# Kernel optimization log

Measured on AMD Instinct MI355X. Metric: run time of the kernel, lower is better.

Reference implementation:

```python
import jax, jax.numpy as jnp
import numpy as np

B, N, OBS, H, S, A, K = 65536, 10, 64, 50, 10, 2, 2  # batch, agents, obs_dim, hidden, comm symbols, actions, k_steps
NEG = -1e9


def setup_inputs() -> dict:
    key = jax.random.key(0)
    ks = jax.random.split(key, 12)
    def lin(k, fan_in, shape):
        return (jax.random.uniform(k, shape, jnp.float32, -1.0, 1.0) / np.sqrt(fan_in).astype(np.float32))
    IN_F = H + S + H  # hidden + comm + skip(h0) = 110
    return {
        "obs": jax.random.normal(ks[0], (B, N, OBS), jnp.float32),
        "mask": jnp.ones((B, N), jnp.float32),
        "W_enc": lin(ks[1], OBS, (OBS, H)),
        "b_enc": lin(ks[2], OBS, (H,)),
        "W_f": lin(ks[3], IN_F, (K, IN_F, H)),
        "b_f": lin(ks[4], IN_F, (K, H)),
        "W_comm": lin(ks[5], H, (H, S)),
        "b_comm": lin(ks[6], H, (S,)),
        "W_pi": lin(ks[7], H, (H, A)),
        "b_pi": lin(ks[8], H, (A,)),
        "W_v": lin(ks[9], H, (H, 1)),
        "b_v": lin(ks[10], H, (1,)),
    }


def reference(obs, mask, W_enc, b_enc, W_f, b_f, W_comm, b_comm, W_pi, b_pi, W_v, b_v):
    mask3 = mask[..., None]                      # [B,N,1]
    h0 = jnp.tanh(obs @ W_enc + b_enc)           # [B,N,H]
    h = h0
    comm_logp = jnp.zeros(obs.shape[:2], obs.dtype)  # [B,N]
    c = jnp.zeros((*obs.shape[:2], S), obs.dtype)
    for i in range(K):  # k_steps is small & static
        comm_logits = h @ W_comm + b_comm        # [B,N,S]
        masked = jnp.where(mask3 == 0, NEG, comm_logits)
        logp = jax.nn.log_softmax(masked, axis=-1)
        w = jnp.argmax(masked, axis=-1)          # greedy symbol per agent [B,N]
        comm_logp = comm_logp + jnp.take_along_axis(logp, w[..., None], axis=-1)[..., 0] * mask
        w_onehot = jax.nn.one_hot(w, S, dtype=obs.dtype)  # [B,N,S]
        # bag-of-words OR aggregation across agents, broadcast back to every agent
        c = jnp.clip(jnp.sum(w_onehot, axis=1, keepdims=True), 0.0, 1.0)  # [B,1,S]
        c = jnp.broadcast_to(c, w_onehot.shape)  # [B,N,S]
        inp = jnp.concatenate([h, c, h0], axis=-1)  # [B,N,H+S+H]
        h = jnp.tanh(inp @ W_f[i] + b_f[i])
    logits = h @ W_pi + b_pi                      # [B,N,A]
    logits = jnp.where(mask3 == 0, NEG, logits)
    baseline = (h @ W_v + b_v)[..., 0] * mask     # [B,N]
    return logits, baseline, comm_logp, c
```

## Files before the change

kernel.cpp:

```cpp
#include <hip/hip_runtime.h>
#include <math.h>

#define NAGENT 10
#define OBS_D  64
#define HID    50
#define NSYM   10
#define NACT   2
#define NEGV   (-1e9f)

#define BPB 6
#define TPB 64
#define AG  (BPB * NAGENT)

#define LD 52

#define OFF_WC0  3328
#define OFF_W1S  5928
#define OFF_W1H  8528
#define OFF_WC0c 11128
#define OFF_W1c  11648
#define NPREP    (234 * LD)

__device__ __forceinline__ float fast_tanh(float x) {
  float xc = fminf(15.f, fmaxf(-15.f, x));
  float e  = __expf(2.f * xc);
  return __fdividef(e - 1.f, e + 1.f);
}

__global__ void prep_weights(const float* __restrict__ W_enc,
                             const float* __restrict__ W_f,
                             float* __restrict__ ws) {
  int i = blockIdx.x * blockDim.x + threadIdx.x;
  if (i >= NPREP) return;
  int j = i % LD;
  int r = i / LD;
  float v = 0.f;
  if (j < HID) {
    if      (r <  64)                { v = W_enc[r*HID + j]; }
    else if (r < 114) { int k=r-64;    v = W_f[k*HID + j] + W_f[(60+k)*HID + j]; }
    else if (r < 164) { int k=r-114;   v = W_f[(110+60+k)*HID + j]; }
    else if (r < 214) { int k=r-164;   v = W_f[(110+k)*HID + j]; }
    else if (r < 224) { int s=r-214;   v = W_f[(50+s)*HID + j]; }
    else              { int s=r-224;   v = W_f[(110+50+s)*HID + j]; }
  }
  ws[i] = v;
}

__device__ __forceinline__ int comm_pick(float cl[NSYM], float mk, float& clp) {
  #pragma unroll
  for (int s = 0; s < NSYM; s++) cl[s] = (mk == 0.f) ? NEGV : cl[s];
  int w = 0; float best = cl[0];
  #pragma unroll
  for (int s = 1; s < NSYM; s++) { bool b = cl[s] > best; best = b ? cl[s] : best; w = b ? s : w; }
  float se = 0.f;
  #pragma unroll
  for (int s = 0; s < NSYM; s++) se += __expf(cl[s] - best);
  clp += (-__logf(se)) * mk;
  return w;
}

__global__ __launch_bounds__(TPB, 4) void policy_kernel(
    const float* __restrict__ obs,
    const float* __restrict__ mask,
    const float* __restrict__ b_enc,
    const float* __restrict__ b_f,
    const float* __restrict__ W_comm,
    const float* __restrict__ b_comm,
    const float* __restrict__ W_pi,
    const float* __restrict__ b_pi,
    const float* __restrict__ W_v,
    const float* __restrict__ b_v,
    const float* __restrict__ wsP,
    float* __restrict__ out,
    int B)
{
  __shared__ float hbuf[AG * 51];
  const int t   = threadIdx.x;
  const int be0 = blockIdx.x * BPB;
  const int nbe = min(BPB, B - be0);
  const int nag = nbe * NAGENT;
  const bool act = (t < nag);
  const int bel = t / NAGENT;
  const long long NA = (long long)B * NAGENT;
  const long long g  = (long long)be0 * NAGENT + t;
  const long long gc = act ? g : (NA - 1);
  const int sl = act ? t : 0;

  const float* WencP = wsP;
  const float* WC0   = wsP + OFF_WC0;
  const float* W1S   = wsP + OFF_W1S;
  const float* W1H   = wsP + OFF_W1H;
  const float* WC0c  = wsP + OFF_WC0c;
  const float* W1c   = wsP + OFF_W1c;

  const float mk = mask[gc];

  float acc[HID];
  #pragma unroll
  for (int j = 0; j < HID; j++) acc[j] = b_enc[j];
  {
    const float4* o4 = (const float4*)(obs + gc * OBS_D);
    #pragma unroll 2
    for (int k4 = 0; k4 < OBS_D / 4; k4++) {
      float4 v = o4[k4];
      const float* wr = &WencP[k4 * 4 * LD];
      #pragma unroll
      for (int j = 0; j < HID; j++) acc[j] = fmaf(v.x, wr[j], acc[j]);
      #pragma unroll
      for (int j = 0; j < HID; j++) acc[j] = fmaf(v.y, wr[LD + j], acc[j]);
      #pragma unroll
      for (int j = 0; j < HID; j++) acc[j] = fmaf(v.z, wr[2 * LD + j], acc[j]);
      #pragma unroll
      for (int j = 0; j < HID; j++) acc[j] = fmaf(v.w, wr[3 * LD + j], acc[j]);
    }
  }

  float cl[NSYM];
  #pragma unroll
  for (int s = 0; s < NSYM; s++) cl[s] = b_comm[s];
  if (act) {
    float* myh = &hbuf[t * 51];
    #pragma unroll
    for (int j = 0; j < HID; j++) {
      float h = fast_tanh(acc[j]);
      myh[j] = h;
      const float* wc = &W_comm[j * NSYM];
      #pragma unroll
      for (int s = 0; s < NSYM; s++) cl[s] = fmaf(h, wc[s], cl[s]);
    }
  }

  float clp = 0.f;

  int w = comm_pick(cl, mk, clp);
  const int sh = bel * NAGENT;
  float c_reg[NSYM];
  #pragma unroll
  for (int s = 0; s < NSYM; s++) {
    unsigned long long b = __ballot(w == s);
    c_reg[s] = ((b >> sh) & 0x3FFULL) ? 1.f : 0.f;
  }

  float pre1[HID];
  #pragma unroll
  for (int j = 0; j < HID; j++) acc[j]  = b_f[j];
  #pragma unroll
  for (int j = 0; j < HID; j++) pre1[j] = b_f[HID + j];
  {
    const float* myh = &hbuf[sl * 51];
    #pragma unroll 2
    for (int k = 0; k < HID; k++) {
      float x = myh[k];
      const float* w0 = &WC0[k * LD];
      const float* w1 = &W1S[k * LD];
      #pragma unroll
      for (int j = 0; j < HID; j++) acc[j]  = fmaf(x, w0[j], acc[j]);
      #pragma unroll
      for (int j = 0; j < HID; j++) pre1[j] = fmaf(x, w1[j], pre1[j]);
    }
  }
  #pragma unroll
  for (int s = 0; s < NSYM; s++) {
    float cv = c_reg[s];
    const float* wr = &WC0c[s * LD];
    #pragma unroll
    for (int j = 0; j < HID; j++) acc[j] = fmaf(cv, wr[j], acc[j]);
  }

  #pragma unroll
  for (int s = 0; s < NSYM; s++) cl[s] = b_comm[s];
  if (act) {
    float* myh = &hbuf[t * 51];
    #pragma unroll
    for (int j = 0; j < HID; j++) {
      float h = fast_tanh(acc[j]);
      myh[j] = h;
      const float* wc = &W_comm[j * NSYM];
      #pragma unroll
      for (int s = 0; s < NSYM; s++) cl[s] = fmaf(h, wc[s], cl[s]);
    }
  }

  w = comm_pick(cl, mk, clp);
  #pragma unroll
  for (int s = 0; s < NSYM; s++) {
    unsigned long long b = __ballot(w == s);
    c_reg[s] = ((b >> sh) & 0x3FFULL) ? 1.f : 0.f;
  }

  #pragma unroll
  for (int s = 0; s < NSYM; s++) {
    float cv = c_reg[s];
    const float* wr = &W1c[s * LD];
    #pragma unroll
    for (int j = 0; j < HID; j++) pre1[j] = fmaf(cv, wr[j], pre1[j]);
  }
  {
    const float* myh = &hbuf[sl * 51];
    #pragma unroll 2
    for (int k = 0; k < HID; k++) {
      float x = myh[k];
      const float* wr = &W1H[k * LD];
      #pragma unroll
      for (int j = 0; j < HID; j++) pre1[j] = fmaf(x, wr[j], pre1[j]);
    }
  }

  float l0 = b_pi[0], l1 = b_pi[1], bv = b_v[0];
  #pragma unroll
  for (int j = 0; j < HID; j++) {
    float h = fast_tanh(pre1[j]);
    l0 = fmaf(h, W_pi[j * NACT + 0], l0);
    l1 = fmaf(h, W_pi[j * NACT + 1], l1);
    bv = fmaf(h, W_v[j], bv);
  }

  if (act) {
    float2* o2 = (float2*)out;
    o2[g] = make_float2((mk == 0.f) ? NEGV : l0, (mk == 0.f) ? NEGV : l1);
    out[NA * 2 + g] = bv * mk;
    out[NA * 3 + g] = clp;
    float2* c2 = (float2*)(out + NA * 4);
    const long long cb = g * (NSYM / 2);
    #pragma unroll
    for (int s = 0; s < NSYM / 2; s++)
      c2[cb + s] = make_float2(c_reg[2 * s], c_reg[2 * s + 1]);
  }
}

extern "C" void kernel_launch(void* const* d_in, const int* in_sizes, int n_in,
                              void* d_out, int out_size, void* d_ws, size_t ws_size,
                              hipStream_t stream) {
  const float* obs    = (const float*)d_in[0];
  const float* mask   = (const float*)d_in[1];
  const float* W_enc  = (const float*)d_in[2];
  const float* b_enc  = (const float*)d_in[3];
  const float* W_f    = (const float*)d_in[4];
  const float* b_f    = (const float*)d_in[5];
  const float* W_comm = (const float*)d_in[6];
  const float* b_comm = (const float*)d_in[7];
  const float* W_pi   = (const float*)d_in[8];
  const float* b_pi   = (const float*)d_in[9];
  const float* W_v    = (const float*)d_in[10];
  const float* b_v    = (const float*)d_in[11];
  float* out = (float*)d_out;
  float* ws  = (float*)d_ws;

  const int B = in_sizes[0] / (NAGENT * OBS_D);

  hipLaunchKernelGGL(prep_weights, dim3((NPREP + 255) / 256), dim3(256), 0, stream,
                     W_enc, W_f, ws);

  const int grid = (B + BPB - 1) / BPB;
  hipLaunchKernelGGL(policy_kernel, dim3(grid), dim3(TPB), 0, stream,
                     obs, mask, b_enc, b_f, W_comm, b_comm, W_pi, b_pi, W_v, b_v,
                     ws, out, B);
}
```

Before: 535.1 us.

## Keep hidden state in registers, stash partial pre-activation in LDS, pad W_comm

The hidden vector h now stays in registers instead of going through shared memory. The partial second-layer pre-activation (h0 contribution) is computed early and parked in LDS, so only one 50-wide accumulator is live at a time. W_comm is re-laid out with padded rows in the workspace, and the obs loads are batched into 8 float4 per half. This is meant to cut LDS round trips and register pressure from holding two accumulators at once. In exchange it adds a block sync and fully unrolled loops, which could raise code size or spill.

After: 1.641 ms. 207% more time.

```diff
diff --git a/kernel.cpp b/kernel.cpp
--- a/kernel.cpp
+++ b/kernel.cpp
@@ -12,14 +12,16 @@
 #define TPB 64
 #define AG  (BPB * NAGENT)
 
-#define LD 52
+#define LD  52
+#define CLD 12
 
 #define OFF_WC0  3328
 #define OFF_W1S  5928
 #define OFF_W1H  8528
 #define OFF_WC0c 11128
 #define OFF_W1c  11648
-#define NPREP    (234 * LD)
+#define OFF_WCM  12168
+#define NPREP    (OFF_WCM + HID * CLD)
 
 __device__ __forceinline__ float fast_tanh(float x) {
   float xc = fminf(15.f, fmaxf(-15.f, x));
@@ -29,21 +31,27 @@
 
 __global__ void prep_weights(const float* __restrict__ W_enc,
                              const float* __restrict__ W_f,
+                             const float* __restrict__ W_comm,
                              float* __restrict__ ws) {
   int i = blockIdx.x * blockDim.x + threadIdx.x;
   if (i >= NPREP) return;
-  int j = i % LD;
-  int r = i / LD;
-  float v = 0.f;
-  if (j < HID) {
-    if      (r <  64)                { v = W_enc[r*HID + j]; }
-    else if (r < 114) { int k=r-64;    v = W_f[k*HID + j] + W_f[(60+k)*HID + j]; }
-    else if (r < 164) { int k=r-114;   v = W_f[(110+60+k)*HID + j]; }
-    else if (r < 214) { int k=r-164;   v = W_f[(110+k)*HID + j]; }
-    else if (r < 224) { int s=r-214;   v = W_f[(50+s)*HID + j]; }
-    else              { int s=r-224;   v = W_f[(110+50+s)*HID + j]; }
-  }
-  ws[i] = v;
+  if (i < OFF_WCM) {
+    int j = i % LD;
+    int r = i / LD;
+    float v = 0.f;
+    if (j < HID) {
+      if      (r <  64)                { v = W_enc[r*HID + j]; }
+      else if (r < 114) { int k=r-64;    v = W_f[k*HID + j] + W_f[(60+k)*HID + j]; }
+      else if (r < 164) { int k=r-114;   v = W_f[(110+60+k)*HID + j]; }
+      else if (r < 214) { int k=r-164;   v = W_f[(110+k)*HID + j]; }
+      else if (r < 224) { int s=r-214;   v = W_f[(50+s)*HID + j]; }
+      else              { int s=r-224;   v = W_f[(110+50+s)*HID + j]; }
+    }
+    ws[i] = v;
+  } else {
+    int r = (i - OFF_WCM) / CLD, j = (i - OFF_WCM) % CLD;
+    ws[i] = (j < NSYM) ? W_comm[r*NSYM + j] : 0.f;
+  }
 }
 
 __device__ __forceinline__ int comm_pick(float cl[NSYM], float mk, float& clp) {
@@ -64,7 +72,6 @@
     const float* __restrict__ mask,
     const float* __restrict__ b_enc,
     const float* __restrict__ b_f,
-    const float* __restrict__ W_comm,
     const float* __restrict__ b_comm,
     const float* __restrict__ W_pi,
     const float* __restrict__ b_pi,
@@ -74,7 +81,7 @@
     float* __restrict__ out,
     int B)
 {
-  __shared__ float hbuf[AG * 51];
+  __shared__ float stash[AG * 51];
   const int t   = threadIdx.x;
   const int be0 = blockIdx.x * BPB;
   const int nbe = min(BPB, B - be0);
@@ -85,6 +92,7 @@
   const long long g  = (long long)be0 * NAGENT + t;
   const long long gc = act ? g : (NA - 1);
   const int sl = act ? t : 0;
+  const int sh = bel * NAGENT;
 
   const float* WencP = wsP;
   const float* WC0   = wsP + OFF_WC0;
@@ -92,127 +100,146 @@
   const float* W1H   = wsP + OFF_W1H;
   const float* WC0c  = wsP + OFF_WC0c;
   const float* W1c   = wsP + OFF_W1c;
+  const float* WCM   = wsP + OFF_WCM;
 
   const float mk = mask[gc];
-
-  float acc[HID];
-  #pragma unroll
-  for (int j = 0; j < HID; j++) acc[j] = b_enc[j];
-  {
+  float h[HID];
+
+  {
+    float acc[HID];
+    #pragma unroll
+    for (int j = 0; j < HID; j++) acc[j] = b_enc[j];
     const float4* o4 = (const float4*)(obs + gc * OBS_D);
-    #pragma unroll 2
-    for (int k4 = 0; k4 < OBS_D / 4; k4++) {
-      float4 v = o4[k4];
-      const float* wr = &WencP[k4 * 4 * LD];
-      #pragma unroll
-      for (int j = 0; j < HID; j++) acc[j] = fmaf(v.x, wr[j], acc[j]);
-      #pragma unroll
-      for (int j = 0; j < HID; j++) acc[j] = fmaf(v.y, wr[LD + j], acc[j]);
-      #pragma unroll
-      for (int j = 0; j < HID; j++) acc[j] = fmaf(v.z, wr[2 * LD + j], acc[j]);
-      #pragma unroll
-      for (int j = 0; j < HID; j++) acc[j] = fmaf(v.w, wr[3 * LD + j], acc[j]);
-    }
-  }
-
-  float cl[NSYM];
-  #pragma unroll
-  for (int s = 0; s < NSYM; s++) cl[s] = b_comm[s];
-  if (act) {
-    float* myh = &hbuf[t * 51];
-    #pragma unroll
-    for (int j = 0; j < HID; j++) {
-      float h = fast_tanh(acc[j]);
-      myh[j] = h;
-      const float* wc = &W_comm[j * NSYM];
-      #pragma unroll
-      for (int s = 0; s < NSYM; s++) cl[s] = fmaf(h, wc[s], cl[s]);
-    }
+    #pragma unroll
+    for (int half = 0; half < 2; half++) {
+      float4 ob[8];
+      #pragma unroll
+      for (int q = 0; q < 8; q++) ob[q] = o4[half * 8 + q];
+      #pragma unroll
+      for (int q = 0; q < 8; q++) {
+        const float* wr = &WencP[(half * 32 + q * 4) * LD];
+        #pragma unroll
+        for (int j = 0; j < HID; j++) acc[j] = fmaf(ob[q].x, wr[j], acc[j]);
+        #pragma unroll
+        for (int j = 0; j < HID; j++) acc[j] = fmaf(ob[q].y, wr[LD + j], acc[j]);
+        #pragma unroll
+        for (int j = 0; j < HID; j++) acc[j] = fmaf(ob[q].z, wr[2 * LD + j], acc[j]);
+        #pragma unroll
+        for (int j = 0; j < HID; j++) acc[j] = fmaf(ob[q].w, wr[3 * LD + j], acc[j]);
+      }
+    }
+    #pragma unroll
+    for (int j = 0; j < HID; j++) h[j] = fast_tanh(acc[j]);
   }
 
   float clp = 0.f;
-
-  int w = comm_pick(cl, mk, clp);
-  const int sh = bel * NAGENT;
   float c_reg[NSYM];
+  int w;
+  {
+    float cl[NSYM];
+    #pragma unroll
+    for (int s = 0; s < NSYM; s++) cl[s] = b_comm[s];
+    #pragma unroll
+    for (int k = 0; k < HID; k++) {
+      float x = h[k];
+      const float* wr = &WCM[k * CLD];
+      #pragma unroll
+      for (int s = 0; s < NSYM; s++) cl[s] = fmaf(x, wr[s], cl[s]);
+    }
+    w = comm_pick(cl, mk, clp);
+  }
   #pragma unroll
   for (int s = 0; s < NSYM; s++) {
     unsigned long long b = __ballot(w == s);
     c_reg[s] = ((b >> sh) & 0x3FFULL) ? 1.f : 0.f;
   }
 
-  float pre1[HID];
-  #pragma unroll
-  for (int j = 0; j < HID; j++) acc[j]  = b_f[j];
-  #pragma unroll
-  for (int j = 0; j < HID; j++) pre1[j] = b_f[HID + j];
-  {
-    const float* myh = &hbuf[sl * 51];
-    #pragma unroll 2
-    for (int k = 0; k < HID; k++) {
-      float x = myh[k];
-      const float* w0 = &WC0[k * LD];
-      const float* w1 = &W1S[k * LD];
-      #pragma unroll
-      for (int j = 0; j < HID; j++) acc[j]  = fmaf(x, w0[j], acc[j]);
-      #pragma unroll
-      for (int j = 0; j < HID; j++) pre1[j] = fmaf(x, w1[j], pre1[j]);
-    }
-  }
-  #pragma unroll
-  for (int s = 0; s < NSYM; s++) {
-    float cv = c_reg[s];
-    const float* wr = &WC0c[s * LD];
-    #pragma unroll
-    for (int j = 0; j < HID; j++) acc[j] = fmaf(cv, wr[j], acc[j]);
-  }
-
-  #pragma unroll
-  for (int s = 0; s < NSYM; s++) cl[s] = b_comm[s];
-  if (act) {
-    float* myh = &hbuf[t * 51];
-    #pragma unroll
-    for (int j = 0; j < HID; j++) {
-      float h = fast_tanh(acc[j]);
-      myh[j] = h;
-      const float* wc = &W_comm[j * NSYM];
-      #pragma unroll
-      for (int s = 0; s < NSYM; s++) cl[s] = fmaf(h, wc[s], cl[s]);
-    }
-  }
-
-  w = comm_pick(cl, mk, clp);
+  {
+    float pre1[HID];
+    #pragma unroll
+    for (int j = 0; j < HID; j++) pre1[j] = b_f[HID + j];
+    #pragma unroll
+    for (int k = 0; k < HID; k++) {
+      float x = h[k];
+      const float* wr = &W1S[k * LD];
+      #pragma unroll
+      for (int j = 0; j < HID; j++) pre1[j] = fmaf(x, wr[j], pre1[j]);
+    }
+    if (act) {
+      #pragma unroll
+      for (int j = 0; j < HID; j++) stash[t * 51 + j] = pre1[j];
+    }
+  }
+  __syncthreads();
+
+  {
+    float acc[HID];
+    #pragma unroll
+    for (int j = 0; j < HID; j++) acc[j] = b_f[j];
+    #pragma unroll
+    for (int s = 0; s < NSYM; s++) {
+      float cv = c_reg[s];
+      const float* wr = &WC0c[s * LD];
+      #pragma unroll
+      for (int j = 0; j < HID; j++) acc[j] = fmaf(cv, wr[j], acc[j]);
+    }
+    #pragma unroll
+    for (int k = 0; k < HID; k++) {
+      float x = h[k];
+      const float* wr = &WC0[k * LD];
+      #pragma unroll
+      for (int j = 0; j < HID; j++) acc[j] = fmaf(x, wr[j], acc[j]);
+    }
+    #pragma unroll
+    for (int j = 0; j < HID; j++) h[j] = fast_tanh(acc[j]);
+  }
+
+  {
+    float cl[NSYM];
+    #pragma unroll
+    for (int s = 0; s < NSYM; s++) cl[s] = b_comm[s];
+    #pragma unroll
+    for (int k = 0; k < HID; k++) {
+      float x = h[k];
+      const float* wr = &WCM[k * CLD];
+      #pragma unroll
+      for (int s = 0; s < NSYM; s++) cl[s] = fmaf(x, wr[s], cl[s]);
+    }
+    w = comm_pick(cl, mk, clp);
+  }
   #pragma unroll
   for (int s = 0; s < NSYM; s++) {
     unsigned long long b = __ballot(w == s);
     c_reg[s] = ((b >> sh) & 0x3FFULL) ? 1.f : 0.f;
   }
 
-  #pragma unroll
-  for (int s = 0; s < NSYM; s++) {
-    float cv = c_reg[s];
-    const float* wr = &W1c[s * LD];
-    #pragma unroll
-    for (int j = 0; j < HID; j++) pre1[j] = fmaf(cv, wr[j], pre1[j]);
-  }
-  {
-    const float* myh = &hbuf[sl * 51];
-    #pragma unroll 2
-    for (int k = 0; k < HID; k++) {
-      float x = myh[k];
+  float l0, l1, bv;
+  {
+    float pre[HID];
+    #pragma unroll
+    for (int j = 0; j < HID; j++) pre[j] = stash[sl * 51 + j];
+    #pragma unroll
+    for (int s = 0; s < NSYM; s++) {
+      float cv = c_reg[s];
+      const float* wr = &W1c[s * LD];
+      #pragma unroll
+      for (int j = 0; j < HID; j++) pre[j] = fmaf(cv, wr[j], pre[j]);
+    }
+    #pragma unroll
+    for (int k = 0; k < HID; k++) {
+      float x = h[k];
       const float* wr = &W1H[k * LD];
       #pragma unroll
-      for (int j = 0; j < HID; j++) pre1[j] = fmaf(x, wr[j], pre1[j]);
-    }
-  }
-
-  float l0 = b_pi[0], l1 = b_pi[1], bv = b_v[0];
-  #pragma unroll
-  for (int j = 0; j < HID; j++) {
-    float h = fast_tanh(pre1[j]);
-    l0 = fmaf(h, W_pi[j * NACT + 0], l0);
-    l1 = fmaf(h, W_pi[j * NACT + 1], l1);
-    bv = fmaf(h, W_v[j], bv);
+      for (int j = 0; j < HID; j++) pre[j] = fmaf(x, wr[j], pre[j]);
+    }
+    l0 = b_pi[0]; l1 = b_pi[1]; bv = b_v[0];
+    #pragma unroll
+    for (int j = 0; j < HID; j++) {
+      float hh = fast_tanh(pre[j]);
+      l0 = fmaf(hh, W_pi[j * NACT + 0], l0);
+      l1 = fmaf(hh, W_pi[j * NACT + 1], l1);
+      bv = fmaf(hh, W_v[j], bv);
+    }
   }
 
   if (act) {
@@ -249,10 +276,10 @@
   const int B = in_sizes[0] / (NAGENT * OBS_D);
 
   hipLaunchKernelGGL(prep_weights, dim3((NPREP + 255) / 256), dim3(256), 0, stream,
-                     W_enc, W_f, ws);
+                     W_enc, W_f, W_comm, ws);
 
   const int grid = (B + BPB - 1) / BPB;
   hipLaunchKernelGGL(policy_kernel, dim3(grid), dim3(TPB), 0, stream,
-                     obs, mask, b_enc, b_f, W_comm, b_comm, W_pi, b_pi, W_v, b_v,
+                     obs, mask, b_enc, b_f, b_comm, W_pi, b_pi, W_v, b_v,
                      ws, out, B);
 }
```
